# Performance work log

Measured on AMD Instinct MI355X. Metric: run time of the kernel, lower is better.

## Reference

```python
import jax, jax.numpy as jnp
import numpy as np

B = 8192          # batch
NUM_PROTOS = 10   # num_prototypes
NUM_CLASSES = 10
N_PATCHES = 14 * 14  # 196 non-overlapping 2x2 patches of a 28x28 image


def setup_inputs() -> dict:
    key = jax.random.key(0)
    k1, k2, k3 = jax.random.split(key, 3)
    x = jax.random.normal(k1, (B, 784), dtype=jnp.float32)
    prototypes = jax.random.normal(k2, (NUM_PROTOS, 4), dtype=jnp.float32)
    W = jax.random.normal(k3, (NUM_CLASSES, NUM_PROTOS * N_PATCHES), dtype=jnp.float32) * 0.02
    b = jnp.zeros((NUM_CLASSES,), dtype=jnp.float32)
    return {"x": x, "prototypes": prototypes, "W": W, "b": b}


def _features(x, prototypes):
    # x: (B, 784) -> non-overlapping 2x2 patches, row-major within each patch
    bsz = x.shape[0]
    img = x.reshape(bsz, 28, 28)
    patches = img.reshape(bsz, 14, 2, 14, 2).transpose(0, 1, 3, 2, 4).reshape(bsz, N_PATCHES, 4)
    # Quantum kernel: ansatz applies RY(x_i) then RY(-y_i) per wire on |0000>.
    # |0...0> amplitude factorizes over the 4 wires: prod_i cos((x_i - y_i)/2).
    diff = patches[:, :, None, :] - prototypes[None, None, :, :]   # (B, 196, P, 4)
    kern = jnp.abs(jnp.prod(jnp.cos(0.5 * diff), axis=-1))          # (B, 196, P)
    # torch stacks per-prototype then permutes to (B, P, 196) and flattens
    return kern.transpose(0, 2, 1).reshape(bsz, -1)                 # (B, P*196)


def reference(x, prototypes, W, b):
    feats = _features(x, prototypes)
    logits = feats @ W.T + b
    return jax.nn.log_softmax(logits, axis=-1)
```

## Files before the change

### kernel.cpp

```cpp
#include <hip/hip_runtime.h>
#include <math.h>

#define B_ROWS 8192
#define NPROTO 10
#define NCLS   10
#define NPATCH 196

#define TABLE_OFF 0
#define WT2_OFF   128
#define PART_OFF  19776
#define XS_STRIDE 113

typedef float v2f __attribute__((ext_vector_type(2)));

__global__ __launch_bounds__(256) void quanv_prep(
    const float* __restrict__ W, const float* __restrict__ protos,
    float* __restrict__ ws) {
  int idx = blockIdx.x * 256 + threadIdx.x;
  if (idx < NPROTO * 8) {
    int proto = idx >> 3;
    int j = idx & 7;
    float h = 0.5f * protos[proto * 4 + (j & 3)];
    ws[TABLE_OFF + idx] = (j < 4) ? __cosf(h) : __sinf(h);
  }
  if (idx < NPATCH * NPROTO * NCLS) {
    int p     = idx / (NPROTO * NCLS);
    int rem   = idx - p * (NPROTO * NCLS);
    int proto = rem / NCLS;
    int c     = rem - proto * NCLS;
    ws[WT2_OFF + idx] = W[c * (NPROTO * NPATCH) + proto * NPATCH + p];
  }
}

__global__ __launch_bounds__(256, 4) void quanv_main(
    const float* __restrict__ x, const float* __restrict__ ws,
    float* __restrict__ partial) {
  __shared__ float xs[64 * XS_STRIDE];

  const int tid = threadIdx.x;
  const int bx  = blockIdx.x;
  const int pr2 = blockIdx.y;

  {
    const float* src = x + (size_t)bx * 64 * 784 + pr2 * 112;
    for (int i = tid; i < 64 * 28; i += 256) {
      int row = i / 28, quad = i - row * 28;
      float4 v = *(const float4*)(src + (size_t)row * 784 + quad * 4);
      float* d = &xs[row * XS_STRIDE + quad * 4];
      d[0] = v.x; d[1] = v.y; d[2] = v.z; d[3] = v.w;
    }
  }
  __syncthreads();

  const int wid  = __builtin_amdgcn_readfirstlane(tid >> 6);
  const int lane = tid & 63;
  const float* tb  = ws + TABLE_OFF;
  const float* Wt2 = ws + WT2_OFF;
  const float* xr  = &xs[lane * XS_STRIDE];

  v2f acc2[5];
#pragma unroll
  for (int k = 0; k < 5; ++k) acc2[k] = (v2f){0.0f, 0.0f};

  for (int j = 0; j < 7; ++j) {
    int lp  = wid * 7 + j;
    int piL = lp >= 14 ? 1 : 0;
    int pj  = lp - piL * 14;
    int off = piL * 56 + 2 * pj;
    float x0 = xr[off],      x1 = xr[off + 1];
    float x2 = xr[off + 28], x3 = xr[off + 29];
    float s0, c0, s1, c1, s2, c2, s3, c3;
    __sincosf(0.5f * x0, &s0, &c0);
    __sincosf(0.5f * x1, &s1, &c1);
    __sincosf(0.5f * x2, &s2, &c2);
    __sincosf(0.5f * x3, &s3, &c3);
    v2f cv01 = {c0, c1}, cv23 = {c2, c3};
    v2f sv01 = {s0, s1}, sv23 = {s2, s3};

    int p = pr2 * 28 + lp;
    const float* wp = Wt2 + p * (NPROTO * NCLS);
#pragma unroll
    for (int proto = 0; proto < NPROTO; ++proto) {
      const float* t8 = tb + proto * 8;
      v2f tc01 = {t8[0], t8[1]}, tc23 = {t8[2], t8[3]};
      v2f ts01 = {t8[4], t8[5]}, ts23 = {t8[6], t8[7]};
      v2f t01 = __builtin_elementwise_fma(cv01, tc01, sv01 * ts01);
      v2f t23 = __builtin_elementwise_fma(cv23, tc23, sv23 * ts23);
      float q  = fabsf((t01.x * t01.y) * (t23.x * t23.y));
      v2f qq = {q, q};
      const v2f* wv = (const v2f*)(wp + proto * NCLS);
#pragma unroll
      for (int k = 0; k < 5; ++k)
        acc2[k] = __builtin_elementwise_fma(qq, wv[k], acc2[k]);
    }
  }

  __syncthreads();
  {
    float* myred = &xs[(wid * 64 + lane) * 11];
#pragma unroll
    for (int k = 0; k < 5; ++k) {
      myred[2 * k]     = acc2[k].x;
      myred[2 * k + 1] = acc2[k].y;
    }
  }
  __syncthreads();

  for (int i = tid; i < 64 * NCLS; i += 256) {
    int row = i / NCLS, c = i - row * NCLS;
    int o = row * 11 + c;
    float s = xs[o] + xs[704 + o] + xs[1408 + o] + xs[2112 + o];
    partial[((size_t)pr2 * B_ROWS + (size_t)bx * 64 + row) * NCLS + c] = s;
  }
}

__global__ __launch_bounds__(256) void quanv_final(
    const float* __restrict__ partial, const float* __restrict__ bias,
    float* __restrict__ out) {
  int r = blockIdx.x * 256 + threadIdx.x;
  float v[NCLS];
#pragma unroll
  for (int c = 0; c < NCLS; ++c) v[c] = bias[c];
  for (int y = 0; y < 7; ++y) {
    const float* pp = partial + ((size_t)y * B_ROWS + r) * NCLS;
#pragma unroll
    for (int c = 0; c < NCLS; c += 2) {
      float2 t = *(const float2*)(pp + c);
      v[c] += t.x; v[c + 1] += t.y;
    }
  }
  float m = v[0];
#pragma unroll
  for (int c = 1; c < NCLS; ++c) m = fmaxf(m, v[c]);
  float sum = 0.0f;
#pragma unroll
  for (int c = 0; c < NCLS; ++c) sum += __expf(v[c] - m);
  float lse = m + __logf(sum);
#pragma unroll
  for (int c = 0; c < NCLS; ++c) out[r * NCLS + c] = v[c] - lse;
}

extern "C" void kernel_launch(void* const* d_in, const int* in_sizes, int n_in,
                              void* d_out, int out_size, void* d_ws, size_t ws_size,
                              hipStream_t stream) {
  const float* x      = (const float*)d_in[0];
  const float* protos = (const float*)d_in[1];
  const float* W      = (const float*)d_in[2];
  const float* bias   = (const float*)d_in[3];
  float* out = (float*)d_out;
  float* ws  = (float*)d_ws;

  quanv_prep<<<(NPATCH * NPROTO * NCLS + 255) / 256, 256, 0, stream>>>(W, protos, ws);
  quanv_main<<<dim3(B_ROWS / 64, 7), 256, 0, stream>>>(x, ws, ws + PART_OFF);
  quanv_final<<<B_ROWS / 256, 256, 0, stream>>>(ws + PART_OFF, bias, out);
}
```

Measured before the change: 92.83 us.

## Fuse final log-softmax reduction into main kernel via last-block atomic counter

```diff
diff --git a/kernel.cpp b/kernel.cpp
--- a/kernel.cpp
+++ b/kernel.cpp
@@ -9,6 +9,8 @@
 #define TABLE_OFF 0
 #define WT2_OFF   128
 #define PART_OFF  19776
+#define PART_ELEMS (7 * B_ROWS * NCLS)
+#define CNT_OFF   (PART_OFF + PART_ELEMS)
 #define XS_STRIDE 113
 
 typedef float v2f __attribute__((ext_vector_type(2)));
@@ -23,6 +25,7 @@
     float h = 0.5f * protos[proto * 4 + (j & 3)];
     ws[TABLE_OFF + idx] = (j < 4) ? __cosf(h) : __sinf(h);
   }
+  if (idx < 128) ((int*)(ws + CNT_OFF))[idx] = 0;
   if (idx < NPATCH * NPROTO * NCLS) {
     int p     = idx / (NPROTO * NCLS);
     int rem   = idx - p * (NPROTO * NCLS);
@@ -34,8 +37,10 @@
 
 __global__ __launch_bounds__(256, 4) void quanv_main(
     const float* __restrict__ x, const float* __restrict__ ws,
-    float* __restrict__ partial) {
+    float* __restrict__ partial, int* __restrict__ cnt,
+    const float* __restrict__ bias, float* __restrict__ out) {
   __shared__ float xs[64 * XS_STRIDE];
+  __shared__ int amLast;
 
   const int tid = threadIdx.x;
   const int bx  = blockIdx.x;
@@ -112,32 +117,43 @@
     float s = xs[o] + xs[704 + o] + xs[1408 + o] + xs[2112 + o];
     partial[((size_t)pr2 * B_ROWS + (size_t)bx * 64 + row) * NCLS + c] = s;
   }
-}
 
-__global__ __launch_bounds__(256) void quanv_final(
-    const float* __restrict__ partial, const float* __restrict__ bias,
-    float* __restrict__ out) {
-  int r = blockIdx.x * 256 + threadIdx.x;
-  float v[NCLS];
+  __threadfence();
+  __syncthreads();
+  if (tid == 0) amLast = (atomicAdd(&cnt[bx], 1) == 6);
+  __syncthreads();
+  if (amLast) {
+    __threadfence();
+    if (tid < 64) {
+      int row = bx * 64 + tid;
+      float v[NCLS];
 #pragma unroll
-  for (int c = 0; c < NCLS; ++c) v[c] = bias[c];
-  for (int y = 0; y < 7; ++y) {
-    const float* pp = partial + ((size_t)y * B_ROWS + r) * NCLS;
+      for (int c = 0; c < NCLS; c += 2) {
+        float2 bb = *(const float2*)(bias + c);
+        v[c] = bb.x; v[c + 1] = bb.y;
+      }
+      for (int y = 0; y < 7; ++y) {
+        const float* pp = partial + ((size_t)y * B_ROWS + row) * NCLS;
 #pragma unroll
-    for (int c = 0; c < NCLS; c += 2) {
-      float2 t = *(const float2*)(pp + c);
-      v[c] += t.x; v[c + 1] += t.y;
+        for (int c = 0; c < NCLS; c += 2) {
+          float2 t = *(const float2*)(pp + c);
+          v[c] += t.x; v[c + 1] += t.y;
+        }
+      }
+      float m = v[0];
+#pragma unroll
+      for (int c = 1; c < NCLS; ++c) m = fmaxf(m, v[c]);
+      float sum = 0.0f;
+#pragma unroll
+      for (int c = 0; c < NCLS; ++c) sum += __expf(v[c] - m);
+      float lse = m + __logf(sum);
+#pragma unroll
+      for (int c = 0; c < NCLS; c += 2) {
+        float2 o = {v[c] - lse, v[c + 1] - lse};
+        *(float2*)(out + (size_t)row * NCLS + c) = o;
+      }
     }
   }
-  float m = v[0];
-#pragma unroll
-  for (int c = 1; c < NCLS; ++c) m = fmaxf(m, v[c]);
-  float sum = 0.0f;
-#pragma unroll
-  for (int c = 0; c < NCLS; ++c) sum += __expf(v[c] - m);
-  float lse = m + __logf(sum);
-#pragma unroll
-  for (int c = 0; c < NCLS; ++c) out[r * NCLS + c] = v[c] - lse;
 }
 
 extern "C" void kernel_launch(void* const* d_in, const int* in_sizes, int n_in,
@@ -151,6 +167,6 @@
   float* ws  = (float*)d_ws;
 
   quanv_prep<<<(NPATCH * NPROTO * NCLS + 255) / 256, 256, 0, stream>>>(W, protos, ws);
-  quanv_main<<<dim3(B_ROWS / 64, 7), 256, 0, stream>>>(x, ws, ws + PART_OFF);
-  quanv_final<<<B_ROWS / 256, 256, 0, stream>>>(ws + PART_OFF, bias, out);
+  quanv_main<<<dim3(B_ROWS / 64, 7), 256, 0, stream>>>(
+      x, ws, ws + PART_OFF, (int*)(ws + CNT_OFF), bias, out);
 }
```

Measured after the change: 157.5 us. 69.6% more time.

## Fold prep kernel into main kernel, read W directly, reorder loops

Applied to the files above, without the earlier changes.

```diff
diff --git a/kernel.cpp b/kernel.cpp
--- a/kernel.cpp
+++ b/kernel.cpp
@@ -5,41 +5,28 @@
 #define NPROTO 10
 #define NCLS   10
 #define NPATCH 196
+#define WROW   (NPROTO * NPATCH)
 
-#define TABLE_OFF 0
-#define WT2_OFF   128
-#define PART_OFF  19776
+#define PART_OFF  0
 #define XS_STRIDE 113
 
 typedef float v2f __attribute__((ext_vector_type(2)));
 
-__global__ __launch_bounds__(256) void quanv_prep(
-    const float* __restrict__ W, const float* __restrict__ protos,
-    float* __restrict__ ws) {
-  int idx = blockIdx.x * 256 + threadIdx.x;
-  if (idx < NPROTO * 8) {
-    int proto = idx >> 3;
-    int j = idx & 7;
-    float h = 0.5f * protos[proto * 4 + (j & 3)];
-    ws[TABLE_OFF + idx] = (j < 4) ? __cosf(h) : __sinf(h);
-  }
-  if (idx < NPATCH * NPROTO * NCLS) {
-    int p     = idx / (NPROTO * NCLS);
-    int rem   = idx - p * (NPROTO * NCLS);
-    int proto = rem / NCLS;
-    int c     = rem - proto * NCLS;
-    ws[WT2_OFF + idx] = W[c * (NPROTO * NPATCH) + proto * NPATCH + p];
-  }
-}
-
-__global__ __launch_bounds__(256, 4) void quanv_main(
-    const float* __restrict__ x, const float* __restrict__ ws,
-    float* __restrict__ partial) {
+__global__ __launch_bounds__(256) void quanv_main(
+    const float* __restrict__ x, const float* __restrict__ protos,
+    const float* __restrict__ W, float* __restrict__ partial) {
   __shared__ float xs[64 * XS_STRIDE];
+  __shared__ float tbl[80];
 
   const int tid = threadIdx.x;
   const int bx  = blockIdx.x;
   const int pr2 = blockIdx.y;
+
+  if (tid < 80) {
+    int proto = tid >> 3, j = tid & 7;
+    float h = 0.5f * protos[proto * 4 + (j & 3)];
+    tbl[tid] = (j < 4) ? __cosf(h) : __sinf(h);
+  }
 
   {
     const float* src = x + (size_t)bx * 64 * 784 + pr2 * 112;
@@ -54,14 +41,11 @@
 
   const int wid  = __builtin_amdgcn_readfirstlane(tid >> 6);
   const int lane = tid & 63;
-  const float* tb  = ws + TABLE_OFF;
-  const float* Wt2 = ws + WT2_OFF;
-  const float* xr  = &xs[lane * XS_STRIDE];
+  const float* xr = &xs[lane * XS_STRIDE];
+  const int p0 = pr2 * 28 + wid * 7;
 
-  v2f acc2[5];
+  v2f cv01[7], cv23[7], sv01[7], sv23[7];
 #pragma unroll
-  for (int k = 0; k < 5; ++k) acc2[k] = (v2f){0.0f, 0.0f};
-
   for (int j = 0; j < 7; ++j) {
     int lp  = wid * 7 + j;
     int piL = lp >= 14 ? 1 : 0;
@@ -74,24 +58,33 @@
     __sincosf(0.5f * x1, &s1, &c1);
     __sincosf(0.5f * x2, &s2, &c2);
     __sincosf(0.5f * x3, &s3, &c3);
-    v2f cv01 = {c0, c1}, cv23 = {c2, c3};
-    v2f sv01 = {s0, s1}, sv23 = {s2, s3};
+    cv01[j] = (v2f){c0, c1}; cv23[j] = (v2f){c2, c3};
+    sv01[j] = (v2f){s0, s1}; sv23[j] = (v2f){s2, s3};
+  }
 
-    int p = pr2 * 28 + lp;
-    const float* wp = Wt2 + p * (NPROTO * NCLS);
+  v2f acc2[5];
 #pragma unroll
-    for (int proto = 0; proto < NPROTO; ++proto) {
-      const float* t8 = tb + proto * 8;
-      v2f tc01 = {t8[0], t8[1]}, tc23 = {t8[2], t8[3]};
-      v2f ts01 = {t8[4], t8[5]}, ts23 = {t8[6], t8[7]};
-      v2f t01 = __builtin_elementwise_fma(cv01, tc01, sv01 * ts01);
-      v2f t23 = __builtin_elementwise_fma(cv23, tc23, sv23 * ts23);
-      float q  = fabsf((t01.x * t01.y) * (t23.x * t23.y));
+  for (int k = 0; k < 5; ++k) acc2[k] = (v2f){0.0f, 0.0f};
+
+#pragma unroll
+  for (int proto = 0; proto < NPROTO; ++proto) {
+    float4 tc = *(const float4*)&tbl[proto * 8];
+    float4 ts = *(const float4*)&tbl[proto * 8 + 4];
+    v2f tc01 = {tc.x, tc.y}, tc23 = {tc.z, tc.w};
+    v2f ts01 = {ts.x, ts.y}, ts23 = {ts.z, ts.w};
+    const float* wbase = W + proto * NPATCH + p0;
+#pragma unroll
+    for (int j = 0; j < 7; ++j) {
+      v2f t01 = __builtin_elementwise_fma(cv01[j], tc01, sv01[j] * ts01);
+      v2f t23 = __builtin_elementwise_fma(cv23[j], tc23, sv23[j] * ts23);
+      float q = fabsf((t01.x * t01.y) * (t23.x * t23.y));
       v2f qq = {q, q};
-      const v2f* wv = (const v2f*)(wp + proto * NCLS);
+      const float* wq = wbase + j;
 #pragma unroll
-      for (int k = 0; k < 5; ++k)
-        acc2[k] = __builtin_elementwise_fma(qq, wv[k], acc2[k]);
+      for (int k = 0; k < 5; ++k) {
+        v2f wv = {wq[(2 * k) * WROW], wq[(2 * k + 1) * WROW]};
+        acc2[k] = __builtin_elementwise_fma(qq, wv, acc2[k]);
+      }
     }
   }
 
@@ -120,7 +113,10 @@
   int r = blockIdx.x * 256 + threadIdx.x;
   float v[NCLS];
 #pragma unroll
-  for (int c = 0; c < NCLS; ++c) v[c] = bias[c];
+  for (int c = 0; c < NCLS; c += 2) {
+    float2 bb = *(const float2*)(bias + c);
+    v[c] = bb.x; v[c + 1] = bb.y;
+  }
   for (int y = 0; y < 7; ++y) {
     const float* pp = partial + ((size_t)y * B_ROWS + r) * NCLS;
 #pragma unroll
@@ -137,7 +133,10 @@
   for (int c = 0; c < NCLS; ++c) sum += __expf(v[c] - m);
   float lse = m + __logf(sum);
 #pragma unroll
-  for (int c = 0; c < NCLS; ++c) out[r * NCLS + c] = v[c] - lse;
+  for (int c = 0; c < NCLS; c += 2) {
+    float2 o = {v[c] - lse, v[c + 1] - lse};
+    *(float2*)(out + (size_t)r * NCLS + c) = o;
+  }
 }
 
 extern "C" void kernel_launch(void* const* d_in, const int* in_sizes, int n_in,
@@ -150,7 +149,6 @@
   float* out = (float*)d_out;
   float* ws  = (float*)d_ws;
 
-  quanv_prep<<<(NPATCH * NPROTO * NCLS + 255) / 256, 256, 0, stream>>>(W, protos, ws);
-  quanv_main<<<dim3(B_ROWS / 64, 7), 256, 0, stream>>>(x, ws, ws + PART_OFF);
+  quanv_main<<<dim3(B_ROWS / 64, 7), 256, 0, stream>>>(x, protos, W, ws + PART_OFF);
   quanv_final<<<B_ROWS / 256, 256, 0, stream>>>(ws + PART_OFF, bias, out);
 }
```

Measured after the change: 91.81 us. About the same (-1.1%).
